# Kernel tuning notes

Hardware: AMD Instinct MI355X
Metric: run time of the kernel (lower is better)

Reference implementation:

```python
import jax, jax.numpy as jnp
import numpy as np

N, E = 100000, 1600000
X_DIM, H_DIM, G_DIM = 128, 64, 64
Y_REP = H_DIM + G_DIM
N_OUT = 2


def setup_inputs() -> dict:
    key = jax.random.key(0)
    ks = jax.random.split(key, 16)
    features = jax.random.normal(ks[0], (N, X_DIM), dtype=jnp.float32)
    treatments = (jax.random.uniform(ks[1], (N,)) < 0.5).astype(jnp.float32)
    edge_index = jax.random.randint(ks[2], (2, E), 0, N, dtype=jnp.int64)
    s = 1.0 / np.sqrt(X_DIM)
    W_phi = jax.random.uniform(ks[3], (X_DIM, H_DIM), minval=-s, maxval=s, dtype=jnp.float32)
    b_phi = jax.random.uniform(ks[4], (H_DIM,), minval=-s, maxval=s, dtype=jnp.float32)
    sg = 1.0 / np.sqrt(H_DIM)
    W_gnn = jax.random.uniform(ks[5], (H_DIM, G_DIM), minval=-sg, maxval=sg, dtype=jnp.float32)
    b_gnn = jax.random.uniform(ks[6], (G_DIM,), minval=-sg, maxval=sg, dtype=jnp.float32)
    sy = 1.0 / np.sqrt(Y_REP)
    W00 = jax.random.uniform(ks[7], (N_OUT, Y_REP, Y_REP), minval=-sy, maxval=sy, dtype=jnp.float32)
    b00 = jax.random.uniform(ks[8], (N_OUT, Y_REP), minval=-sy, maxval=sy, dtype=jnp.float32)
    W10 = jax.random.uniform(ks[9], (N_OUT, Y_REP, Y_REP), minval=-sy, maxval=sy, dtype=jnp.float32)
    b10 = jax.random.uniform(ks[10], (N_OUT, Y_REP), minval=-sy, maxval=sy, dtype=jnp.float32)
    W01 = jax.random.uniform(ks[11], (Y_REP, 1), minval=-sy, maxval=sy, dtype=jnp.float32)
    b01 = jax.random.uniform(ks[12], (1,), minval=-sy, maxval=sy, dtype=jnp.float32)
    W11 = jax.random.uniform(ks[13], (Y_REP, 1), minval=-sy, maxval=sy, dtype=jnp.float32)
    b11 = jax.random.uniform(ks[14], (1,), minval=-sy, maxval=sy, dtype=jnp.float32)
    return dict(features=features, treatments=treatments, edge_index=edge_index,
                W_phi=W_phi, b_phi=b_phi, W_gnn=W_gnn, b_gnn=b_gnn,
                W00=W00, b00=b00, W10=W10, b10=b10,
                W01=W01, b01=b01, W11=W11, b11=b11)


def gcn_conv(x, edge_index, W, b, n_nodes):
    # PyG GCNConv defaults: add self-loops, symmetric deg^-1/2 normalization, bias.
    h = x @ W  # [N, G]
    loop = jnp.arange(n_nodes, dtype=edge_index.dtype)
    src = jnp.concatenate([edge_index[0], loop])
    dst = jnp.concatenate([edge_index[1], loop])
    deg = jax.ops.segment_sum(jnp.ones_like(dst, dtype=h.dtype), dst, num_segments=n_nodes)
    dinv = jnp.where(deg > 0, jax.lax.rsqrt(deg), 0.0)
    norm = dinv[src] * dinv[dst]  # [E+N]
    msg = h[src] * norm[:, None]  # gather + scale
    return jax.ops.segment_sum(msg, dst, num_segments=n_nodes) + b


def reference(features, treatments, edge_index, W_phi, b_phi, W_gnn, b_gnn,
              W00, b00, W10, b10, W01, b01, W11, b11):
    phi_x = jax.nn.relu(features @ W_phi + b_phi)  # [N, H]
    phi_x_t = treatments[:, None] * phi_x
    rep_gnn = gcn_conv(phi_x_t, edge_index, W_gnn, b_gnn, features.shape[0])  # [N, G]
    # dropout is a no-op in eval mode
    rep_post = jnp.concatenate([phi_x, rep_gnn], axis=1)  # [N, H+G]
    # faithful to the original: each iteration recomputes from rep_post (only last layer matters)
    for i in range(N_OUT):
        y00 = jax.nn.relu(rep_post @ W00[i] + b00[i])
        y10 = jax.nn.relu(rep_post @ W10[i] + b10[i])
    y0_pred = (y00 @ W01 + b01).reshape(-1)
    y1_pred = (y10 @ W11 + b11).reshape(-1)
    return y1_pred, y0_pred, phi_x
```

## Files before the change

### kernel.cpp

```cpp
#include <hip/hip_runtime.h>
#include <stdint.h>

typedef unsigned short u16;
typedef unsigned int u32;
typedef unsigned long long u64;
typedef long long ll;

#define XD 128
#define HD 64
#define GD 64
#define YREP 128
#define CAP 40
#define FBLK 512

typedef __attribute__((ext_vector_type(8))) short bf16x8;
typedef __attribute__((ext_vector_type(4))) float f32x4;

#define SWT_LD  136
#define SF_LD   136
#define SO_LD   72

__device__ __forceinline__ float b2f(u16 x) { return __uint_as_float(((u32)x) << 16); }
__device__ __forceinline__ u16 f2b(float f) {
    u32 u = __float_as_uint(f);
    return (u16)((u + 0x7fffu + ((u >> 16) & 1u)) >> 16);
}
__device__ __forceinline__ float ldf(const void* p, size_t i, int bf) {
    return bf ? b2f(((const u16*)p)[i]) : ((const float*)p)[i];
}
__device__ __forceinline__ void stf(void* p, size_t i, float v, int bf) {
    if (bf) ((u16*)p)[i] = f2b(v);
    else ((float*)p)[i] = v;
}
__device__ __forceinline__ int ldi(const void* p, size_t i, int w) {
    return w ? (int)((const ll*)p)[i] : ((const int*)p)[i];
}
__device__ __forceinline__ bf16x8 ld_a8(const void* p, size_t off, int bf) {
    if (bf) return *(const bf16x8*)((const u16*)p + off);
    const float* fp = (const float*)p + off;
    bf16x8 a;
    #pragma unroll
    for (int i = 0; i < 8; ++i) a[i] = (short)f2b(fp[i]);
    return a;
}

__global__ __launch_bounds__(256) void prep_kernel(
    const u32* __restrict__ treat_w, const u32* __restrict__ eidx_w,
    const void* __restrict__ treat,
    const void* __restrict__ W00, const void* __restrict__ W10,
    const void* __restrict__ Wgnn,
    int* __restrict__ flags, u32* __restrict__ mask, u32* __restrict__ cnt,
    u32* __restrict__ WF, int N)
{
    __shared__ int sdet[2];
    int tid = threadIdx.x;
    if (tid < 64) {
        bool isbf = false, nzhi = false;
        for (int i = tid; i < 256; i += 64) {
            isbf |= (treat_w[i] == 0x3F803F80u);
            nzhi |= (eidx_w[2 * i + 1] != 0u);
        }
        u64 mb = __ballot(isbf);
        u64 mn = __ballot(nzhi);
        if (tid == 0) {
            sdet[0] = mb ? 1 : 0;
            sdet[1] = mn ? 0 : 1;
            if (blockIdx.x == 0) { flags[0] = sdet[0]; flags[1] = sdet[1]; }
        }
    }
    __syncthreads();
    int bf = sdet[0];

    int row = blockIdx.x * 256 + tid;
    bool t = (row < N) && (ldf(treat, row, bf) > 0.5f);
    u64 m = __ballot(t);
    int lane = tid & 63;
    int wbase = blockIdx.x * 8 + (tid >> 6) * 2;
    if (lane == 0)  mask[wbase]     = (u32)m;
    if (lane == 32) mask[wbase + 1] = (u32)(m >> 32);
    if (row < N) cnt[row] = 0;

    int g = blockIdx.x * 256 + tid;
    if (g < 18432) {
        const void* src;
        size_t soff;
        int gg, NKT, CDIM;
        u32* dst;
        if (g < 8192)       { src = W00;  soff = (size_t)YREP * YREP; gg = g;         NKT = 4; CDIM = 128; dst = WF; }
        else if (g < 16384) { src = W10;  soff = (size_t)YREP * YREP; gg = g - 8192;  NKT = 4; CDIM = 128; dst = WF + 8192; }
        else                { src = Wgnn; soff = 0;                   gg = g - 16384; NKT = 2; CDIM = 64;  dst = WF + 16384; }
        int ep = gg & 3, ln = (gg >> 2) & 63, ctk = gg >> 8;
        int kt = ctk % NKT, ct = ctk / NKT;
        int k = kt * 32 + (ln >> 4) * 8 + 2 * ep;
        int c = ct * 16 + (ln & 15);
        u32 lo = f2b(ldf(src, soff + (size_t)k * CDIM + c, bf));
        u32 hi = f2b(ldf(src, soff + (size_t)(k + 1) * CDIM + c, bf));
        dst[gg] = lo | (hi << 16);
    }
}

__global__ __launch_bounds__(512) void phifill_kernel(
    const void* __restrict__ feat, const void* __restrict__ Wphi,
    const void* __restrict__ bphi, const void* __restrict__ eidx,
    u32* __restrict__ cnt, u32* __restrict__ slot,
    const u32* __restrict__ mask, void* __restrict__ dout,
    const int* __restrict__ flags, int N, int E)
{
    __shared__ u16 sF[128 * SF_LD];
    __shared__ u16 sWT[64 * SWT_LD];
    u16* sOut = sF;

    int bf = flags[0];
    int tid = threadIdx.x;

    if (blockIdx.x < FBLK) {
        int i64 = flags[1];
        int ftid = blockIdx.x * 512 + tid;
        int stride = FBLK * 512;
        int s[8], d[8];
        #pragma unroll
        for (int j = 0; j < 8; ++j) {
            int i = ftid + j * stride;
            if (i < E) {
                s[j] = ldi(eidx, i, i64);
                d[j] = ldi(eidx, (size_t)E + i, i64);
            } else s[j] = -1;
        }
        u32 t[8];
        #pragma unroll
        for (int j = 0; j < 8; ++j)
            t[j] = (s[j] >= 0) ? ((mask[(u32)s[j] >> 5] >> ((u32)s[j] & 31)) & 1u) : 0u;
        u32 p[8];
        #pragma unroll
        for (int j = 0; j < 8; ++j)
            p[j] = (s[j] >= 0) ? atomicAdd(&cnt[d[j]], 0x10000u | t[j]) : 0u;
        #pragma unroll
        for (int j = 0; j < 8; ++j)
            if (s[j] >= 0 && t[j]) {
                u32 q = p[j] & 0xFFFFu;
                if (q < CAP) slot[(size_t)d[j] * CAP + q] = (u32)s[j];
            }
        return;
    }

    int lane = tid & 63;
    int w = tid >> 6;
    int row0 = (blockIdx.x - FBLK) * 128;
    size_t pbase = 2 * (size_t)N;

    if (bf) {
        for (int i = tid; i < 128 * 64; i += 512) {
            int r = i >> 6, k2 = i & 63;
            int row = row0 + r;
            u32 v = (row < N) ? ((const u32*)feat)[(size_t)row * 64 + k2] : 0u;
            ((u32*)sF)[r * (SF_LD / 2) + k2] = v;
        }
    } else {
        for (int i = tid; i < 128 * 64; i += 512) {
            int r = i >> 6, k2 = i & 63;
            int row = row0 + r;
            u32 v = 0;
            if (row < N) {
                const float* fp = (const float*)feat + (size_t)row * XD + 2 * k2;
                v = (u32)f2b(fp[0]) | ((u32)f2b(fp[1]) << 16);
            }
            ((u32*)sF)[r * (SF_LD / 2) + k2] = v;
        }
    }
    {
        int c = tid >> 3, kq = tid & 7;
        #pragma unroll
        for (int j = 0; j < 8; ++j) {
            int k = kq * 16 + 2 * j;
            u32 pk = (u32)f2b(ldf(Wphi, (size_t)k * HD + c, bf))
                   | ((u32)f2b(ldf(Wphi, (size_t)(k + 1) * HD + c, bf)) << 16);
            ((u32*)sWT)[(c * SWT_LD + k) >> 1] = pk;
        }
    }
    __syncthreads();

    f32x4 acc[4];
    #pragma unroll
    for (int ct = 0; ct < 4; ++ct) acc[ct] = (f32x4){0.f, 0.f, 0.f, 0.f};
    int r0 = w * 16;
    #pragma unroll
    for (int kt = 0; kt < 4; ++kt) {
        bf16x8 a = *(const bf16x8*)&sF[(r0 + (lane & 15)) * SF_LD + kt * 32 + (lane >> 4) * 8];
        #pragma unroll
        for (int ct = 0; ct < 4; ++ct) {
            bf16x8 b = *(const bf16x8*)&sWT[(ct * 16 + (lane & 15)) * SWT_LD + kt * 32 + (lane >> 4) * 8];
            acc[ct] = __builtin_amdgcn_mfma_f32_16x16x32_bf16(a, b, acc[ct], 0, 0, 0);
        }
    }
    __syncthreads();

    #pragma unroll
    for (int ct = 0; ct < 4; ++ct) {
        int c = ct * 16 + (lane & 15);
        float bl = ldf(bphi, c, bf);
        #pragma unroll
        for (int j = 0; j < 4; ++j) {
            float y = acc[ct][j] + bl;
            y = y > 0.f ? y : 0.f;
            sOut[(r0 + (lane >> 4) * 4 + j) * SO_LD + c] = f2b(y);
        }
    }
    __syncthreads();

    if (bf) {
        for (int i = tid; i < 128 * 32; i += 512) {
            int r = i >> 5, k2 = i & 31;
            int row = row0 + r;
            if (row < N)
                ((u32*)dout)[(pbase >> 1) + (size_t)row * 32 + k2] = ((u32*)sOut)[r * (SO_LD / 2) + k2];
        }
    } else {
        for (int i = tid; i < 128 * 64; i += 512) {
            int r = i >> 6, c = i & 63;
            int row = row0 + r;
            if (row < N)
                ((float*)dout)[pbase + (size_t)row * HD + c] = b2f(sOut[r * SO_LD + c]);
        }
    }
}

__global__ __launch_bounds__(256) void gather_slot_kernel(
    const void* __restrict__ dout, const u32* __restrict__ cnt,
    const u32* __restrict__ slot, const u32* __restrict__ mask,
    u16* __restrict__ agg, const int* __restrict__ flags, int N)
{
    int bf = flags[0];
    int lane = threadIdx.x & 63;
    int n = (blockIdx.x * 256 + threadIdx.x) >> 6;
    if (n >= N) return;
    size_t pbase = 2 * (size_t)N;
    u32 cn = cnt[n];
    float dvn = rsqrtf((float)(cn >> 16) + 1.0f);
    u32 tb = (mask[(u32)n >> 5] >> ((u32)n & 31)) & 1u;
    float acc = ldf(dout, pbase + (size_t)n * HD + lane, bf) * (dvn * (float)tb);
    u32 kept = cn & 0xFFFFu; if (kept > CAP) kept = CAP;
    const u32* row = &slot[(size_t)n * CAP];
    for (u32 j0 = 0; j0 < kept; j0 += 8) {
        u32 s[8];
        #pragma unroll
        for (int j = 0; j < 8; ++j)
            s[j] = (j0 + j < kept) ? row[j0 + j] : 0xFFFFFFFFu;
        float wg[8];
        #pragma unroll
        for (int j = 0; j < 8; ++j)
            wg[j] = (s[j] != 0xFFFFFFFFu)
                  ? rsqrtf((float)(cnt[s[j]] >> 16) + 1.0f) : 0.f;
        #pragma unroll
        for (int j = 0; j < 8; ++j)
            if (s[j] != 0xFFFFFFFFu)
                acc += ldf(dout, pbase + (size_t)s[j] * HD + lane, bf) * wg[j];
    }
    agg[(size_t)n * HD + lane] = f2b(acc * dvn);
}

__device__ __forceinline__ void head_mfma_phase2(
    const void* __restrict__ dout, const u16* __restrict__ sGnn,
    const u32* __restrict__ WFh,
    const void* __restrict__ bvec,
    const void* __restrict__ Wlin, float blin,
    size_t yoff, int row0, int N, int lane, int w, int bf,
    bool aval, int arow, size_t pbase, void* dst)
{
    f32x4 acc[8];
    #pragma unroll
    for (int ct = 0; ct < 8; ++ct) acc[ct] = (f32x4){0.f, 0.f, 0.f, 0.f};

    #pragma unroll
    for (int kt = 0; kt < 4; ++kt) {
        bf16x8 a;
        if (kt < 2) {
            #pragma unroll
            for (int i = 0; i < 8; ++i) a[i] = 0;
            if (aval) a = ld_a8(dout, pbase + (size_t)arow * HD + kt * 32 + (lane >> 4) * 8, bf);
        } else {
            a = *(const bf16x8*)&sGnn[((w * 2 + (kt - 2)) * 64 + lane) * 8];
        }
        #pragma unroll
        for (int ct = 0; ct < 8; ++ct) {
            bf16x8 b = *(const bf16x8*)&WFh[((ct * 4 + kt) * 64 + lane) * 4];
            acc[ct] = __builtin_amdgcn_mfma_f32_16x16x32_bf16(a, b, acc[ct], 0, 0, 0);
        }
    }
    float p0 = 0.f, p1 = 0.f, p2 = 0.f, p3 = 0.f;
    #pragma unroll
    for (int ct = 0; ct < 8; ++ct) {
        int c = ct * 16 + (lane & 15);
        float bl = ldf(bvec, (size_t)YREP + c, bf);
        float wl = ldf(Wlin, c, bf);
        float y0 = acc[ct][0] + bl; y0 = y0 > 0.f ? y0 : 0.f; p0 += y0 * wl;
        float y1 = acc[ct][1] + bl; y1 = y1 > 0.f ? y1 : 0.f; p1 += y1 * wl;
        float y2 = acc[ct][2] + bl; y2 = y2 > 0.f ? y2 : 0.f; p2 += y2 * wl;
        float y3 = acc[ct][3] + bl; y3 = y3 > 0.f ? y3 : 0.f; p3 += y3 * wl;
    }
    float p[4] = {p0, p1, p2, p3};
    #pragma unroll
    for (int j = 0; j < 4; ++j) {
        #pragma unroll
        for (int m = 8; m >= 1; m >>= 1)
            p[j] += __shfl_xor(p[j], m, 64);
        if ((lane & 15) == 0) {
            int row = row0 + w * 16 + (lane >> 4) * 4 + j;
            if (row < N) stf(dst, yoff + row, p[j] + blin, bf);
        }
    }
}

__global__ __launch_bounds__(512) void head_kernel(
    void* __restrict__ dout, const u16* __restrict__ agg,
    const u32* __restrict__ WF, const void* __restrict__ bgnn,
    const void* __restrict__ b00, const void* __restrict__ b10,
    const void* __restrict__ W01, const void* __restrict__ b01,
    const void* __restrict__ W11, const void* __restrict__ b11,
    const int* __restrict__ flags, int N)
{
    __shared__ u16 sGnn[8192];

    int bf = flags[0];
    int tid = threadIdx.x;
    int lane = tid & 63;
    int w = tid >> 6;
    int l15 = lane & 15;
    int hi = lane >> 4;
    int row0 = blockIdx.x * 128;
    size_t pbase = 2 * (size_t)N;
    int arow = row0 + w * 16 + l15;
    bool aval = arow < N;

    {
        const u32* WgF = WF + 16384;
        f32x4 g[4];
        #pragma unroll
        for (int ct = 0; ct < 4; ++ct) g[ct] = (f32x4){0.f, 0.f, 0.f, 0.f};
        #pragma unroll
        for (int kt = 0; kt < 2; ++kt) {
            bf16x8 a;
            #pragma unroll
            for (int i = 0; i < 8; ++i) a[i] = 0;
            if (aval) a = *(const bf16x8*)&agg[(size_t)arow * HD + kt * 32 + hi * 8];
            #pragma unroll
            for (int ct = 0; ct < 4; ++ct) {
                bf16x8 b = *(const bf16x8*)&WgF[((ct * 2 + kt) * 64 + lane) * 4];
                g[ct] = __builtin_amdgcn_mfma_f32_16x16x32_bf16(a, b, g[ct], 0, 0, 0);
            }
        }
        #pragma unroll
        for (int ct = 0; ct < 4; ++ct) {
            int c = ct * 16 + l15;
            float bg = ldf(bgnn, c, bf);
            int kt2 = c >> 5, hh = (c >> 3) & 3, e = c & 7;
            #pragma unroll
            for (int j = 0; j < 4; ++j) {
                int r = hi * 4 + j;
                sGnn[(((w * 2 + kt2) * 64) + hh * 16 + r) * 8 + e] = f2b(g[ct][j] + bg);
            }
        }
    }
    __syncthreads();

    head_mfma_phase2(dout, sGnn, WF, b00, W01, ldf(b01, 0, bf),
                     (size_t)N, row0, N, lane, w, bf, aval, arow, pbase, dout);
    head_mfma_phase2(dout, sGnn, WF + 8192, b10, W11, ldf(b11, 0, bf),
                     (size_t)0, row0, N, lane, w, bf, aval, arow, pbase, dout);
}

extern "C" void kernel_launch(void* const* d_in, const int* in_sizes, int n_in,
                              void* d_out, int out_size, void* d_ws, size_t ws_size,
                              hipStream_t stream)
{
    const void* feat  = d_in[0];
    const void* treat = d_in[1];
    const void* eidx  = d_in[2];
    const void* Wphi  = d_in[3];
    const void* bphi  = d_in[4];
    const void* Wgnn  = d_in[5];
    const void* bgnn  = d_in[6];
    const void* W00   = d_in[7];
    const void* b00   = d_in[8];
    const void* W10   = d_in[9];
    const void* b10   = d_in[10];
    const void* W01   = d_in[11];
    const void* b01   = d_in[12];
    const void* W11   = d_in[13];
    const void* b11   = d_in[14];

    const int N = in_sizes[1];
    const int E = in_sizes[2] / 2;
    const int NBLK = (N + 127) / 128;
    const int PBLK = (N + 255) / 256;

    char* w = (char*)d_ws;
    size_t off = 0;
    auto alloc = [&](size_t bytes) { void* p = w + off; off += (bytes + 255) & ~(size_t)255; return p; };

    int*   flags = (int*)alloc(256);
    u32*   cnt   = (u32*)alloc((size_t)N * 4);
    u32*   mask  = (u32*)alloc((size_t)PBLK * 8 * 4);
    u32*   WF    = (u32*)alloc((size_t)18432 * 4);
    u32*   slot  = (u32*)alloc((size_t)N * CAP * 4);
    u16*   agg   = (u16*)alloc((size_t)N * HD * 2);

    prep_kernel<<<PBLK, 256, 0, stream>>>(
        (const u32*)treat, (const u32*)eidx, treat, W00, W10, Wgnn,
        flags, mask, cnt, WF, N);

    phifill_kernel<<<FBLK + NBLK, 512, 0, stream>>>(
        feat, Wphi, bphi, eidx, cnt, slot, mask, d_out, flags, N, E);

    gather_slot_kernel<<<(N + 3) / 4, 256, 0, stream>>>(
        d_out, cnt, slot, mask, agg, flags, N);

    head_kernel<<<NBLK, 512, 0, stream>>>(
        d_out, agg, WF, bgnn, b00, b10, W01, b01, W11, b11, flags, N);
}
```

Before: 246.2 us.

## Prepack W_phi into MFMA fragments and load phi GEMM operands directly from global

W_phi is now converted to bf16 MFMA B-fragment layout once in the prep kernel, alongside the other weights. The phi GEMM in phifill reads features straight from global memory into A fragments and prepacked weights straight from the workspace, with no shared-memory staging. Only a small per-wave output buffer stays in LDS, and the block-wide barriers are gone. This cuts LDS use and sync cost and should raise occupancy, but the unstaged, strided global loads for features may coalesce less well.

```diff
diff --git a/kernel.cpp b/kernel.cpp
--- a/kernel.cpp
+++ b/kernel.cpp
@@ -16,8 +16,6 @@
 typedef __attribute__((ext_vector_type(8))) short bf16x8;
 typedef __attribute__((ext_vector_type(4))) float f32x4;
 
-#define SWT_LD  136
-#define SF_LD   136
 #define SO_LD   72
 
 __device__ __forceinline__ float b2f(u16 x) { return __uint_as_float(((u32)x) << 16); }
@@ -48,7 +46,7 @@
     const u32* __restrict__ treat_w, const u32* __restrict__ eidx_w,
     const void* __restrict__ treat,
     const void* __restrict__ W00, const void* __restrict__ W10,
-    const void* __restrict__ Wgnn,
+    const void* __restrict__ Wgnn, const void* __restrict__ Wphi,
     int* __restrict__ flags, u32* __restrict__ mask, u32* __restrict__ cnt,
     u32* __restrict__ WF, int N)
 {
@@ -81,14 +79,15 @@
     if (row < N) cnt[row] = 0;
 
     int g = blockIdx.x * 256 + tid;
-    if (g < 18432) {
+    if (g < 22528) {
         const void* src;
         size_t soff;
         int gg, NKT, CDIM;
         u32* dst;
         if (g < 8192)       { src = W00;  soff = (size_t)YREP * YREP; gg = g;         NKT = 4; CDIM = 128; dst = WF; }
         else if (g < 16384) { src = W10;  soff = (size_t)YREP * YREP; gg = g - 8192;  NKT = 4; CDIM = 128; dst = WF + 8192; }
-        else                { src = Wgnn; soff = 0;                   gg = g - 16384; NKT = 2; CDIM = 64;  dst = WF + 16384; }
+        else if (g < 18432) { src = Wgnn; soff = 0;                   gg = g - 16384; NKT = 2; CDIM = 64;  dst = WF + 16384; }
+        else                { src = Wphi; soff = 0;                   gg = g - 18432; NKT = 4; CDIM = 64;  dst = WF + 18432; }
         int ep = gg & 3, ln = (gg >> 2) & 63, ctk = gg >> 8;
         int kt = ctk % NKT, ct = ctk / NKT;
         int k = kt * 32 + (ln >> 4) * 8 + 2 * ep;
@@ -100,15 +99,13 @@
 }
 
 __global__ __launch_bounds__(512) void phifill_kernel(
-    const void* __restrict__ feat, const void* __restrict__ Wphi,
+    const void* __restrict__ feat, const u32* __restrict__ WF,
     const void* __restrict__ bphi, const void* __restrict__ eidx,
     u32* __restrict__ cnt, u32* __restrict__ slot,
     const u32* __restrict__ mask, void* __restrict__ dout,
     const int* __restrict__ flags, int N, int E)
 {
-    __shared__ u16 sF[128 * SF_LD];
-    __shared__ u16 sWT[64 * SWT_LD];
-    u16* sOut = sF;
+    __shared__ u16 sOut[128 * SO_LD];
 
     int bf = flags[0];
     int tid = threadIdx.x;
@@ -145,78 +142,52 @@
 
     int lane = tid & 63;
     int w = tid >> 6;
+    int l15 = lane & 15;
+    int hi = lane >> 4;
     int row0 = (blockIdx.x - FBLK) * 128;
+    int r0 = w * 16;
     size_t pbase = 2 * (size_t)N;
-
-    if (bf) {
-        for (int i = tid; i < 128 * 64; i += 512) {
-            int r = i >> 6, k2 = i & 63;
-            int row = row0 + r;
-            u32 v = (row < N) ? ((const u32*)feat)[(size_t)row * 64 + k2] : 0u;
-            ((u32*)sF)[r * (SF_LD / 2) + k2] = v;
-        }
-    } else {
-        for (int i = tid; i < 128 * 64; i += 512) {
-            int r = i >> 6, k2 = i & 63;
-            int row = row0 + r;
-            u32 v = 0;
-            if (row < N) {
-                const float* fp = (const float*)feat + (size_t)row * XD + 2 * k2;
-                v = (u32)f2b(fp[0]) | ((u32)f2b(fp[1]) << 16);
-            }
-            ((u32*)sF)[r * (SF_LD / 2) + k2] = v;
-        }
-    }
-    {
-        int c = tid >> 3, kq = tid & 7;
-        #pragma unroll
-        for (int j = 0; j < 8; ++j) {
-            int k = kq * 16 + 2 * j;
-            u32 pk = (u32)f2b(ldf(Wphi, (size_t)k * HD + c, bf))
-                   | ((u32)f2b(ldf(Wphi, (size_t)(k + 1) * HD + c, bf)) << 16);
-            ((u32*)sWT)[(c * SWT_LD + k) >> 1] = pk;
-        }
-    }
-    __syncthreads();
+    int arow = row0 + r0 + l15;
+    bool aval = arow < N;
+    const u32* WFp = WF + 18432;
 
     f32x4 acc[4];
     #pragma unroll
     for (int ct = 0; ct < 4; ++ct) acc[ct] = (f32x4){0.f, 0.f, 0.f, 0.f};
-    int r0 = w * 16;
     #pragma unroll
     for (int kt = 0; kt < 4; ++kt) {
-        bf16x8 a = *(const bf16x8*)&sF[(r0 + (lane & 15)) * SF_LD + kt * 32 + (lane >> 4) * 8];
+        bf16x8 a;
+        #pragma unroll
+        for (int i = 0; i < 8; ++i) a[i] = 0;
+        if (aval) a = ld_a8(feat, (size_t)arow * XD + kt * 32 + hi * 8, bf);
         #pragma unroll
         for (int ct = 0; ct < 4; ++ct) {
-            bf16x8 b = *(const bf16x8*)&sWT[(ct * 16 + (lane & 15)) * SWT_LD + kt * 32 + (lane >> 4) * 8];
+            bf16x8 b = *(const bf16x8*)&WFp[((ct * 4 + kt) * 64 + lane) * 4];
             acc[ct] = __builtin_amdgcn_mfma_f32_16x16x32_bf16(a, b, acc[ct], 0, 0, 0);
         }
     }
-    __syncthreads();
-
     #pragma unroll
     for (int ct = 0; ct < 4; ++ct) {
-        int c = ct * 16 + (lane & 15);
+        int c = ct * 16 + l15;
         float bl = ldf(bphi, c, bf);
         #pragma unroll
         for (int j = 0; j < 4; ++j) {
             float y = acc[ct][j] + bl;
             y = y > 0.f ? y : 0.f;
-            sOut[(r0 + (lane >> 4) * 4 + j) * SO_LD + c] = f2b(y);
-        }
-    }
-    __syncthreads();
-
+            sOut[(r0 + hi * 4 + j) * SO_LD + c] = f2b(y);
+        }
+    }
     if (bf) {
-        for (int i = tid; i < 128 * 32; i += 512) {
-            int r = i >> 5, k2 = i & 31;
+        for (int i = lane; i < 16 * 32; i += 64) {
+            int r = r0 + (i >> 5), k2 = i & 31;
             int row = row0 + r;
             if (row < N)
-                ((u32*)dout)[(pbase >> 1) + (size_t)row * 32 + k2] = ((u32*)sOut)[r * (SO_LD / 2) + k2];
+                ((u32*)dout)[(pbase >> 1) + (size_t)row * 32 + k2] =
+                    ((u32*)sOut)[r * (SO_LD / 2) + k2];
         }
     } else {
-        for (int i = tid; i < 128 * 64; i += 512) {
-            int r = i >> 6, c = i & 63;
+        for (int i = lane; i < 16 * 64; i += 64) {
+            int r = r0 + (i >> 6), c = i & 63;
             int row = row0 + r;
             if (row < N)
                 ((float*)dout)[pbase + (size_t)row * HD + c] = b2f(sOut[r * SO_LD + c]);
@@ -400,16 +371,16 @@
     int*   flags = (int*)alloc(256);
     u32*   cnt   = (u32*)alloc((size_t)N * 4);
     u32*   mask  = (u32*)alloc((size_t)PBLK * 8 * 4);
-    u32*   WF    = (u32*)alloc((size_t)18432 * 4);
+    u32*   WF    = (u32*)alloc((size_t)22528 * 4);
     u32*   slot  = (u32*)alloc((size_t)N * CAP * 4);
     u16*   agg   = (u16*)alloc((size_t)N * HD * 2);
 
     prep_kernel<<<PBLK, 256, 0, stream>>>(
-        (const u32*)treat, (const u32*)eidx, treat, W00, W10, Wgnn,
+        (const u32*)treat, (const u32*)eidx, treat, W00, W10, Wgnn, Wphi,
         flags, mask, cnt, WF, N);
 
     phifill_kernel<<<FBLK + NBLK, 512, 0, stream>>>(
-        feat, Wphi, bphi, eidx, cnt, slot, mask, d_out, flags, N, E);
+        feat, WF, bphi, eidx, cnt, slot, mask, d_out, flags, N, E);
 
     gather_slot_kernel<<<(N + 3) / 4, 256, 0, stream>>>(
         d_out, cnt, slot, mask, agg, flags, N);
```

New measurement: 242.9 us. Within noise of the previous version (-1.3%).
